# Kernel optimization log

Measured on AMD Instinct MI355X. Metric: run time of the kernel, lower is better.

The kernel has to match this reference:

```python
import jax, jax.numpy as jnp
import numpy as np

N_TOKEN = 267735
CUTOFF_ENDS = [0, 20000, 40000, 200000, N_TOKEN]
DIV_VAL = 4
D_MODEL = 1024
N_HEAD = 16
D_HEAD = 64
D_INNER = 4096
N_LAYER = 4
QLEN = 512
MLEN = 512
BSZ = 4
EPS = 1e-5


def setup_inputs() -> dict:
    key = jax.random.key(0)
    ks = iter(jax.random.split(key, 40))
    std = 0.02
    inp = {}
    inp["input_ids"] = jax.random.randint(next(ks), (BSZ, QLEN), 0, N_TOKEN)
    inp["mems"] = jax.random.normal(next(ks), (N_LAYER, MLEN, BSZ, D_MODEL), jnp.float32) * std
    # adaptive embedding tables + projections (div_val=4 buckets)
    for i in range(4):
        n = CUTOFF_ENDS[i + 1] - CUTOFF_ENDS[i]
        d = D_MODEL // DIV_VAL ** i
        inp[f"emb{i}"] = jax.random.normal(next(ks), (n, d), jnp.float32) * std
        inp[f"proj{i}"] = jax.random.normal(next(ks), (d, D_MODEL), jnp.float32) * std
    L = N_LAYER
    inp["qkv_w"] = jax.random.normal(next(ks), (L, D_MODEL, 3 * N_HEAD * D_HEAD), jnp.float32) * std
    inp["r_net_w"] = jax.random.normal(next(ks), (L, D_MODEL, N_HEAD * D_HEAD), jnp.float32) * std
    inp["o_w"] = jax.random.normal(next(ks), (L, N_HEAD * D_HEAD, D_MODEL), jnp.float32) * std
    inp["r_w_bias"] = jax.random.normal(next(ks), (L, N_HEAD, D_HEAD), jnp.float32) * std
    inp["r_r_bias"] = jax.random.normal(next(ks), (L, N_HEAD, D_HEAD), jnp.float32) * std
    inp["ln1_g"] = jnp.ones((L, D_MODEL), jnp.float32)
    inp["ln1_b"] = jnp.zeros((L, D_MODEL), jnp.float32)
    inp["ff_w1"] = jax.random.normal(next(ks), (L, D_MODEL, D_INNER), jnp.float32) * std
    inp["ff_b1"] = jnp.zeros((L, D_INNER), jnp.float32)
    inp["ff_w2"] = jax.random.normal(next(ks), (L, D_INNER, D_MODEL), jnp.float32) * std
    inp["ff_b2"] = jnp.zeros((L, D_MODEL), jnp.float32)
    inp["ln2_g"] = jnp.ones((L, D_MODEL), jnp.float32)
    inp["ln2_b"] = jnp.zeros((L, D_MODEL), jnp.float32)
    return inp


def _layer_norm(x, g, b):
    m = x.mean(-1, keepdims=True)
    v = ((x - m) ** 2).mean(-1, keepdims=True)
    return (x - m) * jax.lax.rsqrt(v + EPS) * g + b


def _rel_shift(x):
    # x: (qlen, klen, bsz, n_head)
    q, k, b, n = x.shape
    x = jnp.pad(x, ((0, 0), (1, 0), (0, 0), (0, 0)))
    x = x.reshape(k + 1, q, b, n)[1:]
    return x.reshape(q, k, b, n)


def _adaptive_embed(flat_ids, tables_projs):
    emb = jnp.zeros((flat_ids.shape[0], D_MODEL), jnp.float32)
    for i, (tab, proj) in enumerate(tables_projs):
        l, r = CUTOFF_ENDS[i], CUTOFF_ENDS[i + 1]
        mask = (flat_ids >= l) & (flat_ids < r)
        idx = jnp.clip(flat_ids - l, 0, r - l - 1)
        emb = emb + jnp.where(mask[:, None], tab[idx] @ proj, 0.0)
    return emb * (D_MODEL ** 0.5)


def _forward(input_ids, mems, tables_projs, qkv_w, r_net_w, o_w, r_w_bias, r_r_bias,
             ln1_g, ln1_b, ff_w1, ff_b1, ff_w2, ff_b2, ln2_g, ln2_b):
    ids = input_ids.T  # (qlen, bsz)
    word_emb = _adaptive_embed(ids.reshape(-1), tables_projs).reshape(QLEN, BSZ, D_MODEL)

    klen = MLEN + QLEN
    # masked positions == 1: future tokens only (strictly upper triangular over the q part)
    dec_attn_mask = jnp.concatenate(
        [jnp.zeros((QLEN, MLEN), jnp.float32), jnp.triu(jnp.ones((QLEN, QLEN), jnp.float32), 1)], axis=1
    )[:, :, None, None]  # (qlen, klen, 1, 1)

    pos_seq = jnp.arange(klen - 1, -1, -1, dtype=jnp.float32)
    inv_freq = 1.0 / (10000.0 ** (jnp.arange(0, D_MODEL, 2, dtype=jnp.float32) / D_MODEL))
    sin_inp = pos_seq[:, None] * inv_freq[None, :]
    pos_emb = jnp.concatenate([jnp.sin(sin_inp), jnp.cos(sin_inp)], axis=-1)  # (klen, d_model)

    scale = 1.0 / (D_HEAD ** 0.5)
    h = word_emb
    for l in range(N_LAYER):
        cat = jnp.concatenate([mems[l], h], axis=0)              # (klen, bsz, d)
        w_heads = cat @ qkv_w[l]                                  # (klen, bsz, 3*nh*dh)
        wq, wk, wv = jnp.split(w_heads, 3, axis=-1)
        q = wq[-QLEN:].reshape(QLEN, BSZ, N_HEAD, D_HEAD)
        k = wk.reshape(klen, BSZ, N_HEAD, D_HEAD)
        v = wv.reshape(klen, BSZ, N_HEAD, D_HEAD)
        rk = (pos_emb @ r_net_w[l]).reshape(klen, N_HEAD, D_HEAD)
        AC = jnp.einsum('ibnd,jbnd->ijbn', q + r_w_bias[l], k)
        BD = _rel_shift(jnp.einsum('ibnd,jnd->ijbn', q + r_r_bias[l], rk))
        score = (AC + BD) * scale
        score = score * (1.0 - dec_attn_mask) - 1e30 * dec_attn_mask
        prob = jax.nn.softmax(score, axis=1)
        attn_vec = jnp.einsum('ijbn,jbnd->ibnd', prob, v).reshape(QLEN, BSZ, N_HEAD * D_HEAD)
        h = _layer_norm(h + attn_vec @ o_w[l], ln1_g[l], ln1_b[l])
        core = jax.nn.relu(h @ ff_w1[l] + ff_b1[l]) @ ff_w2[l] + ff_b2[l]
        h = _layer_norm(h + core, ln2_g[l], ln2_b[l])
    return jnp.transpose(h, (1, 0, 2))  # (bsz, qlen, d_model)


def reference(input_ids, mems, emb0, proj0, emb1, proj1, emb2, proj2, emb3, proj3,
              qkv_w, r_net_w, o_w, r_w_bias, r_r_bias, ln1_g, ln1_b,
              ff_w1, ff_b1, ff_w2, ff_b2, ln2_g, ln2_b):
    tables_projs = [(emb0, proj0), (emb1, proj1), (emb2, proj2), (emb3, proj3)]
    return _forward(input_ids, mems, tables_projs, qkv_w, r_net_w, o_w, r_w_bias, r_r_bias,
                    ln1_g, ln1_b, ff_w1, ff_b1, ff_w2, ff_b2, ln2_g, ln2_b)
```

## Files before the change

kernel.cpp:

```cpp
#include <hip/hip_runtime.h>
#include <hip/hip_bf16.h>

typedef __attribute__((ext_vector_type(8))) short short8;
typedef __attribute__((ext_vector_type(4))) float f32x4;
typedef __hip_bfloat16 bf16;

#define QLEN 512
#define MLEN 512
#define KLEN 1024
#define BSZ  4
#define DM   1024
#define NH   16
#define DH   64
#define DI   4096
#define NL   4
#define KEMB 1408

__device__ __forceinline__ void gload16(const bf16* g, const void* l) {
  __builtin_amdgcn_global_load_lds(
      (const __attribute__((address_space(1))) void*)g,
      (__attribute__((address_space(3))) void*)l, 16, 0, 0);
}

__device__ __forceinline__ bf16 bits2bf(short s) { bf16 h; *(short*)&h = s; return h; }

__global__ __launch_bounds__(256) void embA_kernel(
    const int* __restrict__ ids,
    const float* __restrict__ e0, const float* __restrict__ e1,
    const float* __restrict__ e2, const float* __restrict__ e3,
    bf16* __restrict__ Aemb)
{
  const int t = blockIdx.x;
  const int q = t >> 2, b = t & 3;
  const int id = ids[b * QLEN + q];
  const float* tab; int d, off, koff;
  if (id < 20000)       { tab = e0; d = 1024; off = 0;      koff = 0; }
  else if (id < 40000)  { tab = e1; d = 256;  off = 20000;  koff = 1024; }
  else if (id < 200000) { tab = e2; d = 64;   off = 40000;  koff = 1280; }
  else                  { tab = e3; d = 16;   off = 200000; koff = 1344; }
  bf16* row = Aemb + (long)t * KEMB;
  const float* tr = tab + (long)(id - off) * d;
  for (int k = threadIdx.x; k < KEMB; k += 256) {
    const int kk = k - koff;
    float v = 0.f;
    if (kk >= 0 && kk < d) v = tr[kk];
    row[k] = __float2bfloat16(v);
  }
}

__global__ __launch_bounds__(256) void projT_kernel(
    const float* __restrict__ p0, const float* __restrict__ p1,
    const float* __restrict__ p2, const float* __restrict__ p3,
    bf16* __restrict__ out)
{
  __shared__ float t[32][33];
  const int k0 = blockIdx.x * 32, n0 = blockIdx.y * 32;
  const int nx = threadIdx.x & 31, ky = threadIdx.x >> 5;
#pragma unroll
  for (int p = 0; p < 4; ++p) {
    const int k = k0 + ky + p * 8;
    float v = 0.f;
    if (k < 1024)       v = p0[(long)k * 1024 + n0 + nx];
    else if (k < 1280)  v = p1[(long)(k - 1024) * 1024 + n0 + nx];
    else if (k < 1344)  v = p2[(long)(k - 1280) * 1024 + n0 + nx];
    else if (k < 1360)  v = p3[(long)(k - 1344) * 1024 + n0 + nx];
    t[ky + p * 8][nx] = v;
  }
  __syncthreads();
#pragma unroll
  for (int p = 0; p < 4; ++p)
    out[(long)(n0 + ky + p * 8) * KEMB + k0 + nx] = __float2bfloat16(t[nx][ky + p * 8]);
}

__global__ __launch_bounds__(256) void embsum_kernel(const float* __restrict__ part,
                                                     float* __restrict__ h, bf16* __restrict__ cat)
{
  const long i = ((long)blockIdx.x * 256 + threadIdx.x) * 4;
  const float4 a = *(const float4*)(part + i);
  const float4 b = *(const float4*)(part + 2097152 + i);
  float4 s; s.x = a.x + b.x; s.y = a.y + b.y; s.z = a.z + b.z; s.w = a.w + b.w;
  *(float4*)(h + i) = s;
  bf16* cr = cat + (long)2048 * 1024 + i;
  cr[0] = __float2bfloat16(s.x); cr[1] = __float2bfloat16(s.y);
  cr[2] = __float2bfloat16(s.z); cr[3] = __float2bfloat16(s.w);
}

__global__ __launch_bounds__(256) void posemb_kernel(bf16* __restrict__ pe)
{
  const int j = blockIdx.x;
  const float pos = (float)(KLEN - 1 - j);
  for (int i = threadIdx.x; i < DM / 2; i += 256) {
    const float freq = expf(-9.210340371976184f * ((float)(2 * i) / (float)DM));
    const float ang = pos * freq;
    pe[(long)j * DM + i]          = __float2bfloat16(sinf(ang));
    pe[(long)j * DM + DM / 2 + i] = __float2bfloat16(cosf(ang));
  }
}

__global__ __launch_bounds__(256) void wtrans_kernel(const float* __restrict__ in,
                                                     bf16* __restrict__ out, int R, int C)
{
  __shared__ float t[32][33];
  in  += (long)blockIdx.z * R * C;
  out += (long)blockIdx.z * R * C;
  const int c0 = blockIdx.x * 32, r0 = blockIdx.y * 32;
  const int cx = threadIdx.x & 31, ry = threadIdx.x >> 5;
#pragma unroll
  for (int p = 0; p < 4; ++p)
    t[ry + p * 8][cx] = in[(long)(r0 + ry + p * 8) * C + c0 + cx];
  __syncthreads();
#pragma unroll
  for (int p = 0; p < 4; ++p)
    out[(long)(c0 + ry + p * 8) * R + r0 + cx] = __float2bfloat16(t[cx][ry + p * 8]);
}

__global__ __launch_bounds__(256) void memsconv_kernel(const float* __restrict__ mems,
                                                       bf16* __restrict__ cat0)
{
  const long i = ((long)blockIdx.x * 256 + threadIdx.x) * 4;
  const long l = i >> 21, rem = i & ((1 << 21) - 1);
  const float4 v = *(const float4*)(mems + i);
  bf16* dst = cat0 + l * 4194304 + rem;
  dst[0] = __float2bfloat16(v.x); dst[1] = __float2bfloat16(v.y);
  dst[2] = __float2bfloat16(v.z); dst[3] = __float2bfloat16(v.w);
}

template<int BM, int BN>
__global__ __launch_bounds__(256) void gemm_bf16(
    const bf16* __restrict__ A, long aStrB, long aStrN, int lda,
    const bf16* __restrict__ B, long bStrB, long bStrN, int ldb,
    void* __restrict__ C, long cStrB, long cStrN, int ldc,
    int K, float scale, const float* __restrict__ bias, long biasStrB, long biasStrN,
    int flags, int zN, int zSplit, long cSplitStr)
{
  constexpr int RA = BM / 64, RB = BN / 64, FM = BM / 32, FN = BN / 32;
  __shared__ __align__(16) bf16 As[2][BM * 32];
  __shared__ __align__(16) bf16 Bs[2][BN * 32];
  const int zc = blockIdx.z % zSplit, zt = blockIdx.z / zSplit;
  const int zn = zt % zN, zb = zt / zN;
  A += (long)zb * aStrB + (long)zn * aStrN + (long)zc * K;
  B += (long)zb * bStrB + (long)zn * bStrN + (long)zc * K;
  const int tid = threadIdx.x, lane = tid & 63;
  const int w = tid >> 6, wr = w >> 1, wc = w & 1;
  const int m0 = blockIdx.y * BM, n0 = blockIdx.x * BN;
  const int l15 = lane & 15, l4 = lane >> 4;
  const int rowS = tid >> 2;
  const int cbS  = (tid & 3) * 16;
  const int swS  = cbS ^ (((rowS >> 1) & 3) << 4);
  const int wbase = w * 1024;
  const bf16* Ast = A + (size_t)(m0 + rowS) * lda + (swS >> 1);
  const bf16* Bst = B + (size_t)(n0 + rowS) * ldb + (swS >> 1);

#define STAGE_TILE(buf, kk)                                                       \
  {                                                                               \
    _Pragma("unroll")                                                             \
    for (int r = 0; r < RA; ++r)                                                  \
      gload16(Ast + (size_t)(r * 64) * lda + (kk), (char*)As[buf] + r * 4096 + wbase); \
    _Pragma("unroll")                                                             \
    for (int r = 0; r < RB; ++r)                                                  \
      gload16(Bst + (size_t)(r * 64) * ldb + (kk), (char*)Bs[buf] + r * 4096 + wbase); \
  }

  f32x4 acc[FM][FN] = {};
  STAGE_TILE(0, 0)
  asm volatile("s_waitcnt vmcnt(0)" ::: "memory");
  __syncthreads();
  int cur = 0;
  for (int k0 = 0; k0 < K; k0 += 32) {
    if (k0 + 32 < K) {
      if (cur == 0) STAGE_TILE(1, k0 + 32)
      else          STAGE_TILE(0, k0 + 32)
    }
    short8 af[FM], bfr[FN];
#pragma unroll
    for (int f = 0; f < FM; ++f) {
      const int row = wr * (BM / 2) + f * 16 + l15;
      af[f] = *(const short8*)((char*)As[cur] + row * 64 + ((16 * l4) ^ (((row >> 1) & 3) << 4)));
    }
#pragma unroll
    for (int f = 0; f < FN; ++f) {
      const int row = wc * (BN / 2) + f * 16 + l15;
      bfr[f] = *(const short8*)((char*)Bs[cur] + row * 64 + ((16 * l4) ^ (((row >> 1) & 3) << 4)));
    }
#pragma unroll
    for (int fm = 0; fm < FM; ++fm)
#pragma unroll
      for (int fn = 0; fn < FN; ++fn)
        acc[fm][fn] = __builtin_amdgcn_mfma_f32_16x16x32_bf16(af[fm], bfr[fn], acc[fm][fn], 0, 0, 0);
    asm volatile("s_waitcnt vmcnt(0)" ::: "memory");
    __syncthreads();
    cur ^= 1;
  }
#undef STAGE_TILE
  const int outbf = flags & 1, relu = flags & 4;
#pragma unroll
  for (int fm = 0; fm < FM; ++fm) {
#pragma unroll
    for (int fn = 0; fn < FN; ++fn) {
      const int col = n0 + wc * (BN / 2) + fn * 16 + l15;
      const int rw0 = m0 + wr * (BM / 2) + fm * 16 + l4 * 4;
      const float bv = (bias && zc == 0) ? bias[(size_t)zb * biasStrB + (size_t)zn * biasStrN + col] : 0.f;
#pragma unroll
      for (int r = 0; r < 4; ++r) {
        float v = (acc[fm][fn][r] + bv) * scale;
        if (relu) v = fmaxf(v, 0.f);
        const int row = rw0 + r;
        const size_t cOff = (size_t)zb * cStrB + (size_t)zn * cStrN + (size_t)zc * cSplitStr;
        if (outbf) {
          ((bf16*)C + cOff)[(size_t)row * ldc + col] = __float2bfloat16(v);
        } else {
          ((float*)C + cOff)[(size_t)row * ldc + col] = v;
        }
      }
    }
  }
}

__global__ __launch_bounds__(256) void vt_kernel(const bf16* __restrict__ wh,
                                                 bf16* __restrict__ vt, bf16* __restrict__ kb)
{
  const int bn = blockIdx.y, b = bn >> 4, n = bn & 15;
  const int j0 = blockIdx.x * 64;
  __shared__ bf16 t[64][72];
  const bf16* src = wh + (size_t)b * 3072 + 2048 + n * 64;
  const bf16* ksrc = wh + (size_t)b * 3072 + 1024 + n * 64;
  bf16* kdst = kb + (size_t)bn * 65536;
  const int tid = threadIdx.x;
#pragma unroll
  for (int r = 0; r < 16; ++r) {
    const int jl = r * 4 + (tid >> 6), d = tid & 63;
    t[jl][d] = src[(size_t)(j0 + jl) * 12288 + d];
    kdst[(size_t)(j0 + jl) * 64 + d] = ksrc[(size_t)(j0 + jl) * 12288 + d];
  }
  __syncthreads();
  bf16* dst = vt + (size_t)bn * 65536 + (size_t)j0 * 64;
#pragma unroll
  for (int r = 0; r < 16; ++r) {
    const int d = r * 4 + (tid >> 6), j = tid & 63;
    dst[(size_t)d * 64 + j] = t[j][d];
  }
}

__global__ __launch_bounds__(256) void rkpack_kernel(const bf16* __restrict__ rkb,
                                                     bf16* __restrict__ rkn)
{
  const int ln = blockIdx.y, l = ln >> 4, n = ln & 15;
  const int p0 = blockIdx.x * 64;
  const int d = threadIdx.x & 63, pr = threadIdx.x >> 6;
  const bf16* src = rkb + (size_t)l * 1048576 + n * 64 + d;
  bf16* dst = rkn + (size_t)ln * 65536 + d;
#pragma unroll
  for (int r = 0; r < 16; ++r) {
    const int p = p0 + r * 4 + pr;
    dst[(size_t)p * 64] = src[(size_t)p * 1024];
  }
}

__global__ __launch_bounds__(256) void fattn_kernel(
    const bf16* __restrict__ wh,
    const bf16* __restrict__ kb,
    const bf16* __restrict__ rkn_l,
    const bf16* __restrict__ vt,
    const float* __restrict__ rwb,
    const float* __restrict__ rrb,
    float* __restrict__ po, float* __restrict__ pm, float* __restrict__ pl)
{
  const int bn = blockIdx.x, b = bn >> 4, n = bn & 15;
  const int q0 = blockIdx.y * 64;
  const int ck = blockIdx.z;
  const int tid = threadIdx.x, w = tid >> 6, lane = tid & 63;
  const int l15 = lane & 15, l4 = lane >> 4;
  __shared__ bf16 Tl[4][16][84];
  __shared__ bf16 Pl[4][16][72];

  short8 qa[2], qb[2];
  {
    const bf16* qp = wh + (size_t)(2048 + b) * 3072 + (size_t)(q0 + 16 * w + l15) * 12288 + n * 64;
#pragma unroll
    for (int kk = 0; kk < 2; ++kk) {
      const short8 qv = *(const short8*)(qp + kk * 32 + 8 * l4);
      const float* wv = rwb + n * 64 + kk * 32 + 8 * l4;
      const float* rv = rrb + n * 64 + kk * 32 + 8 * l4;
      short8 a, c;
#pragma unroll
      for (int e = 0; e < 8; ++e) {
        const float q = __bfloat162float(bits2bf(qv[e]));
        const bf16 ab = __float2bfloat16((q + wv[e]) * 0.125f);
        const bf16 cb = __float2bfloat16((q + rv[e]) * 0.125f);
        a[e] = *(const short*)&ab;  c[e] = *(const short*)&cb;
      }
      qa[kk] = a; qb[kk] = c;
    }
  }

  const bf16* kbase = kb + (size_t)bn * 65536;
  const bf16* rbase = rkn_l + (size_t)n * 65536;
  const bf16* vbase = vt + (size_t)bn * 65536;
  const int ntiles = 9 + (q0 >> 6);
  const int pb0 = -q0 + 496 - 16 * w;

  f32x4 accO[4] = {};
  float mrow[4] = { -1e30f, -1e30f, -1e30f, -1e30f };
  float lrow[4] = { 0.f, 0.f, 0.f, 0.f };

  for (int t = ck; t < ntiles; t += 4) {
    const int j0 = t * 64;
    f32x4 S[4] = {};
#pragma unroll
    for (int fn = 0; fn < 4; ++fn)
#pragma unroll
      for (int kk = 0; kk < 2; ++kk) {
        const short8 kf = *(const short8*)(kbase + (size_t)(j0 + 16 * fn + l15) * 64 + kk * 32 + 8 * l4);
        S[fn] = __builtin_amdgcn_mfma_f32_16x16x32_bf16(qa[kk], kf, S[fn], 0, 0, 0);
      }
    {
      f32x4 T[5] = {};
#pragma unroll
      for (int ftl = 0; ftl < 5; ++ftl) {
        const int p = pb0 + j0 + 16 * ftl + l15;
#pragma unroll
        for (int kk = 0; kk < 2; ++kk) {
          const short8 rf = *(const short8*)(rbase + (size_t)p * 64 + kk * 32 + 8 * l4);
          T[ftl] = __builtin_amdgcn_mfma_f32_16x16x32_bf16(qb[kk], rf, T[ftl], 0, 0, 0);
        }
      }
#pragma unroll
      for (int ftl = 0; ftl < 5; ++ftl)
#pragma unroll
        for (int r = 0; r < 4; ++r)
          Tl[w][4 * l4 + r][16 * ftl + l15] = __float2bfloat16(T[ftl][r]);
    }
    const bool fullvalid = (j0 + 63) <= (512 + q0);
    float sv[4][4];
#pragma unroll
    for (int fn = 0; fn < 4; ++fn)
#pragma unroll
      for (int r = 0; r < 4; ++r) {
        const int il = 4 * l4 + r;
        const float tshift = __bfloat162float(Tl[w][il][16 * fn + l15 + 15 - il]);
        const float s = S[fn][r] + tshift;
        const bool valid = fullvalid || (j0 + 16 * fn + l15 - 512 <= q0 + 16 * w + il);
        sv[fn][r] = valid ? s : -1e30f;
      }
#pragma unroll
    for (int r = 0; r < 4; ++r) {
      float m4 = fmaxf(fmaxf(sv[0][r], sv[1][r]), fmaxf(sv[2][r], sv[3][r]));
      m4 = fmaxf(m4, __shfl_xor(m4, 1));
      m4 = fmaxf(m4, __shfl_xor(m4, 2));
      m4 = fmaxf(m4, __shfl_xor(m4, 4));
      m4 = fmaxf(m4, __shfl_xor(m4, 8));
      const float mn = fmaxf(mrow[r], m4);
      const float alpha = expf(mrow[r] - mn);
      mrow[r] = mn;
      float ps = 0.f;
#pragma unroll
      for (int fn = 0; fn < 4; ++fn) {
        sv[fn][r] = expf(sv[fn][r] - mn);
        ps += sv[fn][r];
      }
      ps += __shfl_xor(ps, 1);
      ps += __shfl_xor(ps, 2);
      ps += __shfl_xor(ps, 4);
      ps += __shfl_xor(ps, 8);
      lrow[r] = lrow[r] * alpha + ps;
#pragma unroll
      for (int fd = 0; fd < 4; ++fd) accO[fd][r] *= alpha;
    }
#pragma unroll
    for (int fn = 0; fn < 4; ++fn)
#pragma unroll
      for (int r = 0; r < 4; ++r)
        Pl[w][4 * l4 + r][16 * fn + l15] = __float2bfloat16(sv[fn][r]);
    short8 pa[2];
    pa[0] = *(const short8*)&Pl[w][l15][8 * l4];
    pa[1] = *(const short8*)&Pl[w][l15][32 + 8 * l4];
    const bf16* vtile = vbase + (size_t)j0 * 64;
#pragma unroll
    for (int fd = 0; fd < 4; ++fd)
#pragma unroll
      for (int kk = 0; kk < 2; ++kk) {
        const short8 vf = *(const short8*)(vtile + (size_t)(16 * fd + l15) * 64 + kk * 32 + 8 * l4);
        accO[fd] = __builtin_amdgcn_mfma_f32_16x16x32_bf16(pa[kk], vf, accO[fd], 0, 0, 0);
      }
  }
  const int cb = ck * 64 + bn;
  float* pob = po + (size_t)cb * 512 * 64;
#pragma unroll
  for (int fd = 0; fd < 4; ++fd)
#pragma unroll
    for (int r = 0; r < 4; ++r) {
      const int row = q0 + 16 * w + 4 * l4 + r;
      pob[(size_t)row * 64 + 16 * fd + l15] = accO[fd][r];
    }
  if (l15 == 0) {
#pragma unroll
    for (int r = 0; r < 4; ++r) {
      const int row = q0 + 16 * w + 4 * l4 + r;
      pm[(size_t)cb * 512 + row] = mrow[r];
      pl[(size_t)cb * 512 + row] = lrow[r];
    }
  }
}

__global__ __launch_bounds__(256) void fmerge_kernel(
    const float* __restrict__ po, const float* __restrict__ pm,
    const float* __restrict__ pl, bf16* __restrict__ av)
{
  const long i = ((long)blockIdx.x * 256 + threadIdx.x) * 4;
  const long bnq = i >> 6;
  const int d4 = (int)(i & 63);
  const int bn = (int)(bnq >> 9), q = (int)(bnq & 511);
  const int b = bn >> 4, n = bn & 15;
  float mv[4], lv[4];
#pragma unroll
  for (int c = 0; c < 4; ++c) { mv[c] = pm[c * 32768 + bnq]; lv[c] = pl[c * 32768 + bnq]; }
  const float m = fmaxf(fmaxf(mv[0], mv[1]), fmaxf(mv[2], mv[3]));
  float wv[4], den = 0.f;
#pragma unroll
  for (int c = 0; c < 4; ++c) { wv[c] = expf(mv[c] - m); den += wv[c] * lv[c]; }
  const float inv = 1.f / den;
  float4 o = { 0.f, 0.f, 0.f, 0.f };
#pragma unroll
  for (int c = 0; c < 4; ++c) {
    const float4 oc = *(const float4*)(po + (size_t)c * 2097152 + bnq * 64 + d4);
    o.x += wv[c] * oc.x; o.y += wv[c] * oc.y; o.z += wv[c] * oc.z; o.w += wv[c] * oc.w;
  }
  bf16* dst = av + (size_t)(q * 4 + b) * 1024 + n * 64 + d4;
  dst[0] = __float2bfloat16(o.x * inv);
  dst[1] = __float2bfloat16(o.y * inv);
  dst[2] = __float2bfloat16(o.z * inv);
  dst[3] = __float2bfloat16(o.w * inv);
}

__global__ __launch_bounds__(256) void add_ln_kernel(
    float* __restrict__ h,
    const float* __restrict__ x0, const float* __restrict__ x1,
    const float* __restrict__ g, const float* __restrict__ bb, bf16* __restrict__ cat)
{
  float* hr = h + (long)blockIdx.x * DM;
  const long o = (long)blockIdx.x * DM;
  bf16* cr = cat + (long)(2048 + blockIdx.x) * DM;
  const int tid = threadIdx.x;
  __shared__ float red[256];
  float v0 = hr[tid]       + x0[o + tid]       + x1[o + tid];
  float v1 = hr[tid + 256] + x0[o + tid + 256] + x1[o + tid + 256];
  float v2 = hr[tid + 512] + x0[o + tid + 512] + x1[o + tid + 512];
  float v3 = hr[tid + 768] + x0[o + tid + 768] + x1[o + tid + 768];
  red[tid] = v0 + v1 + v2 + v3; __syncthreads();
  for (int off = 128; off; off >>= 1) { if (tid < off) red[tid] += red[tid + off]; __syncthreads(); }
  const float mean = red[0] * (1.f / DM); __syncthreads();
  const float d0 = v0 - mean, d1 = v1 - mean, d2 = v2 - mean, d3 = v3 - mean;
  red[tid] = d0 * d0 + d1 * d1 + d2 * d2 + d3 * d3; __syncthreads();
  for (int off = 128; off; off >>= 1) { if (tid < off) red[tid] += red[tid + off]; __syncthreads(); }
  const float inv = rsqrtf(red[0] * (1.f / DM) + 1e-5f);
  const float o0 = d0 * inv * g[tid]       + bb[tid];
  const float o1 = d1 * inv * g[tid + 256] + bb[tid + 256];
  const float o2 = d2 * inv * g[tid + 512] + bb[tid + 512];
  const float o3 = d3 * inv * g[tid + 768] + bb[tid + 768];
  hr[tid]       = o0;  cr[tid]       = __float2bfloat16(o0);
  hr[tid + 256] = o1;  cr[tid + 256] = __float2bfloat16(o1);
  hr[tid + 512] = o2;  cr[tid + 512] = __float2bfloat16(o2);
  hr[tid + 768] = o3;  cr[tid + 768] = __float2bfloat16(o3);
}

__global__ __launch_bounds__(256) void out_kernel(const float* __restrict__ h, float* __restrict__ out)
{
  const int t = blockIdx.x, q = t >> 2, b = t & 3;
  const float* hr = h + (long)t * DM;
  float* orow = out + ((long)b * QLEN + q) * DM;
  for (int s = 0; s < 4; ++s) orow[threadIdx.x + 256 * s] = hr[threadIdx.x + 256 * s];
}

extern "C" void kernel_launch(void* const* d_in, const int* in_sizes, int n_in,
                              void* d_out, int out_size, void* d_ws, size_t ws_size,
                              hipStream_t stream)
{
  const int*   ids  = (const int*)d_in[0];
  const float* mems = (const float*)d_in[1];
  const float* e0 = (const float*)d_in[2]; const float* p0 = (const float*)d_in[3];
  const float* e1 = (const float*)d_in[4]; const float* p1 = (const float*)d_in[5];
  const float* e2 = (const float*)d_in[6]; const float* p2 = (const float*)d_in[7];
  const float* e3 = (const float*)d_in[8]; const float* p3 = (const float*)d_in[9];
  const float* qkvw = (const float*)d_in[10];
  const float* rnet = (const float*)d_in[11];
  const float* ow   = (const float*)d_in[12];
  const float* rwb  = (const float*)d_in[13];
  const float* rrb  = (const float*)d_in[14];
  const float* ln1g = (const float*)d_in[15];
  const float* ln1b = (const float*)d_in[16];
  const float* fw1  = (const float*)d_in[17];
  const float* fb1  = (const float*)d_in[18];
  const float* fw2  = (const float*)d_in[19];
  const float* fb2  = (const float*)d_in[20];
  const float* ln2g = (const float*)d_in[21];
  const float* ln2b = (const float*)d_in[22];
  float* out = (float*)d_out;

  char* p = (char*)d_ws;
  float* h    = (float*)p;            p += (size_t)2048 * 1024 * 4;
  bf16*  cat0 = (bf16*)p;             p += (size_t)5 * 4096 * 1024 * 2;
  bf16*  pe   = (bf16*)p;             p += (size_t)1024 * 1024 * 2;
  bf16*  rkb  = (bf16*)p;             p += (size_t)4 * 1024 * 1024 * 2;
  bf16*  rkn  = (bf16*)p;             p += (size_t)(4 * 16 * 1024 * 64 + 8192) * 2;
  bf16*  wh   = (bf16*)p;             p += (size_t)4096 * 3072 * 2;
  bf16*  vt   = (bf16*)p;             p += (size_t)64 * 64 * 1024 * 2;
  bf16*  kb   = (bf16*)p;             p += (size_t)64 * 1024 * 64 * 2;
  bf16*  qkvT = (bf16*)p;             p += (size_t)4 * 3072 * 1024 * 2;
  bf16*  rnT  = (bf16*)p;             p += (size_t)4 * 1024 * 1024 * 2;
  bf16*  oT   = (bf16*)p;             p += (size_t)4 * 1024 * 1024 * 2;
  bf16*  f1T  = (bf16*)p;             p += (size_t)4 * 4096 * 1024 * 2;
  bf16*  f2T  = (bf16*)p;             p += (size_t)4 * 4096 * 1024 * 2;
  bf16*  mid  = (bf16*)p;
  float* partE= (float*)p;
  p += (size_t)4 * 16 * 512 * 1024 * 2;
  bf16*  Aemb = (bf16*)p;
  bf16*  projT= (bf16*)(p + (size_t)2048 * KEMB * 2);
  float* partP= (float*)p;
  float* po   = (float*)p;
  float* pm   = (float*)(p + (size_t)32 * 1024 * 1024);
  float* pl   = (float*)(p + (size_t)33 * 1024 * 1024);
  p += (size_t)4 * 16 * 512 * 1024 * 2;
  bf16*  av   = (bf16*)p;             p += (size_t)2048 * 1024 * 2;

  embA_kernel<<<2048, 256, 0, stream>>>(ids, e0, e1, e2, e3, Aemb);
  projT_kernel<<<dim3(KEMB / 32, 32), 256, 0, stream>>>(p0, p1, p2, p3, projT);
  gemm_bf16<128, 64><<<dim3(16, 16, 2), 256, 0, stream>>>(
      Aemb, 0, 0, KEMB, projT, 0, 0, KEMB, partE, 0, 0, 1024,
      KEMB / 2, 32.f, nullptr, 0, 0, 0, 1, 2, 2097152);
  embsum_kernel<<<2048, 256, 0, stream>>>(partE, h, cat0);
  posemb_kernel<<<1024, 256, 0, stream>>>(pe);
  memsconv_kernel<<<8192, 256, 0, stream>>>(mems, cat0);

  wtrans_kernel<<<dim3(96, 32, 4), 256, 0, stream>>>(qkvw, qkvT, DM, 3072);
  wtrans_kernel<<<dim3(32, 32, 4), 256, 0, stream>>>(rnet, rnT, DM, DM);
  wtrans_kernel<<<dim3(32, 32, 4), 256, 0, stream>>>(ow, oT, DM, DM);
  wtrans_kernel<<<dim3(128, 32, 4), 256, 0, stream>>>(fw1, f1T, DM, DI);
  wtrans_kernel<<<dim3(32, 128, 4), 256, 0, stream>>>(fw2, f2T, DI, DM);

  gemm_bf16<128, 128><<<dim3(8, 8, 4), 256, 0, stream>>>(
      pe, 0, 0, 1024, rnT, 1048576, 0, 1024, rkb, 1048576, 0, 1024,
      1024, 1.f, nullptr, 0, 0, 1, 1, 1, 0);
  rkpack_kernel<<<dim3(16, 64), 256, 0, stream>>>(rkb, rkn);

  for (int l = 0; l < NL; ++l) {
    bf16* catl = cat0 + (size_t)l * 4194304;
    gemm_bf16<128, 128><<<dim3(24, 32, 1), 256, 0, stream>>>(
        catl, 0, 0, 1024, qkvT + (size_t)l * 3145728, 0, 0, 1024, wh, 0, 0, 3072,
        1024, 1.f, nullptr, 0, 0, 1, 1, 1, 0);

    vt_kernel<<<dim3(16, 64), 256, 0, stream>>>(wh, vt, kb);

    fattn_kernel<<<dim3(64, 8, 4), 256, 0, stream>>>(
        wh, kb, rkn + (size_t)l * 1048576, vt,
        rwb + l * NH * DH, rrb + l * NH * DH, po, pm, pl);
    fmerge_kernel<<<2048, 256, 0, stream>>>(po, pm, pl, av);

    gemm_bf16<128, 64><<<dim3(16, 16, 2), 256, 0, stream>>>(
        av, 0, 0, 1024, oT + (size_t)l * 1048576, 0, 0, 1024, partP, 0, 0, 1024,
        512, 1.f, nullptr, 0, 0, 0, 1, 2, 2097152);
    add_ln_kernel<<<2048, 256, 0, stream>>>(h, partP, partP + 2097152,
                                            ln1g + l * DM, ln1b + l * DM, catl);

    gemm_bf16<128, 128><<<dim3(32, 16, 1), 256, 0, stream>>>(
        catl + (size_t)2048 * 1024, 0, 0, 1024, f1T + (size_t)l * 4194304, 0, 0, 1024,
        mid, 0, 0, 4096, 1024, 1.f, fb1 + (size_t)l * DI, 0, 0, 1 | 4, 1, 1, 0);
    gemm_bf16<128, 64><<<dim3(16, 16, 2), 256, 0, stream>>>(
        mid, 0, 0, 4096, f2T + (size_t)l * 4194304, 0, 0, 4096, partP, 0, 0, 1024,
        2048, 1.f, fb2 + (size_t)l * DM, 0, 0, 0, 1, 2, 2097152);
    add_ln_kernel<<<2048, 256, 0, stream>>>(h, partP, partP + 2097152,
                                            ln2g + l * DM, ln2b + l * DM,
                                            cat0 + (size_t)(l + 1) * 4194304);
  }

  out_kernel<<<2048, 256, 0, stream>>>(h, out);
}
```

Measured before the change: 1.159 ms.

## Stage K, V and relative-position tiles in swizzled LDS for attention kernel

The attention kernel now cooperatively loads each 64-row K tile, V tile and 128-row relative-position key tile into LDS with direct global-to-LDS loads and an XOR swizzle. All four waves then read their MFMA operands from shared memory instead of each wave loading them from global memory. This is meant to cut redundant global/L2 traffic, since the four waves previously reloaded the same K/V rows and overlapping R rows. It adds two block barriers and a full vmcnt wait per tile with no double-buffering, so load latency is exposed rather than overlapped.

```diff
diff --git a/kernel.cpp b/kernel.cpp
--- a/kernel.cpp
+++ b/kernel.cpp
@@ -270,6 +270,9 @@
   const int ck = blockIdx.z;
   const int tid = threadIdx.x, w = tid >> 6, lane = tid & 63;
   const int l15 = lane & 15, l4 = lane >> 4;
+  __shared__ __align__(16) bf16 Ks[64 * 64];
+  __shared__ __align__(16) bf16 Vs[64 * 64];
+  __shared__ __align__(16) bf16 Rs[128 * 64];
   __shared__ bf16 Tl[4][16][84];
   __shared__ bf16 Pl[4][16][72];
 
@@ -299,28 +302,58 @@
   const int ntiles = 9 + (q0 >> 6);
   const int pb0 = -q0 + 496 - 16 * w;
 
+  const int stRow0 = tid >> 3;
+  const int stColb = (tid & 7) * 16;
+  const int wbase = w * 1024;
+  const int srd = (l15 & 7) << 4;
+
   f32x4 accO[4] = {};
   float mrow[4] = { -1e30f, -1e30f, -1e30f, -1e30f };
   float lrow[4] = { 0.f, 0.f, 0.f, 0.f };
 
   for (int t = ck; t < ntiles; t += 4) {
     const int j0 = t * 64;
+    const int pstart = j0 - q0 + 448;
+    __syncthreads();
+    {
+#pragma unroll
+      for (int r = 0; r < 2; ++r) {
+        const int row = r * 32 + stRow0;
+        gload16(kbase + (size_t)(j0 + row) * 64 + ((stColb ^ ((row & 7) << 4)) >> 1),
+                (char*)Ks + r * 4096 + wbase);
+      }
+#pragma unroll
+      for (int r = 0; r < 2; ++r) {
+        const int row = r * 32 + stRow0;
+        gload16(vbase + (size_t)j0 * 64 + (size_t)row * 64 + ((stColb ^ ((row & 7) << 4)) >> 1),
+                (char*)Vs + r * 4096 + wbase);
+      }
+#pragma unroll
+      for (int r = 0; r < 4; ++r) {
+        const int row = r * 32 + stRow0;
+        gload16(rbase + (size_t)(pstart + row) * 64 + ((stColb ^ ((row & 7) << 4)) >> 1),
+                (char*)Rs + r * 4096 + wbase);
+      }
+    }
+    asm volatile("s_waitcnt vmcnt(0)" ::: "memory");
+    __syncthreads();
+
     f32x4 S[4] = {};
 #pragma unroll
     for (int fn = 0; fn < 4; ++fn)
 #pragma unroll
       for (int kk = 0; kk < 2; ++kk) {
-        const short8 kf = *(const short8*)(kbase + (size_t)(j0 + 16 * fn + l15) * 64 + kk * 32 + 8 * l4);
+        const short8 kf = *(const short8*)((char*)Ks + (16 * fn + l15) * 128 + ((kk * 64 + 16 * l4) ^ srd));
         S[fn] = __builtin_amdgcn_mfma_f32_16x16x32_bf16(qa[kk], kf, S[fn], 0, 0, 0);
       }
     {
       f32x4 T[5] = {};
 #pragma unroll
       for (int ftl = 0; ftl < 5; ++ftl) {
-        const int p = pb0 + j0 + 16 * ftl + l15;
+        const int rrow = (3 - w) * 16 + 16 * ftl + l15;
 #pragma unroll
         for (int kk = 0; kk < 2; ++kk) {
-          const short8 rf = *(const short8*)(rbase + (size_t)p * 64 + kk * 32 + 8 * l4);
+          const short8 rf = *(const short8*)((char*)Rs + rrow * 128 + ((kk * 64 + 16 * l4) ^ srd));
           T[ftl] = __builtin_amdgcn_mfma_f32_16x16x32_bf16(qb[kk], rf, T[ftl], 0, 0, 0);
         }
       }
@@ -374,12 +407,11 @@
     short8 pa[2];
     pa[0] = *(const short8*)&Pl[w][l15][8 * l4];
     pa[1] = *(const short8*)&Pl[w][l15][32 + 8 * l4];
-    const bf16* vtile = vbase + (size_t)j0 * 64;
 #pragma unroll
     for (int fd = 0; fd < 4; ++fd)
 #pragma unroll
       for (int kk = 0; kk < 2; ++kk) {
-        const short8 vf = *(const short8*)(vtile + (size_t)(16 * fd + l15) * 64 + kk * 32 + 8 * l4);
+        const short8 vf = *(const short8*)((char*)Vs + (16 * fd + l15) * 128 + ((kk * 64 + 16 * l4) ^ srd));
         accO[fd] = __builtin_amdgcn_mfma_f32_16x16x32_bf16(pa[kk], vf, accO[fd], 0, 0, 0);
       }
   }
```

New measurement: 980.8 us. -15.3%, faster.

## Stage K, V and R tiles in swizzled double-buffered LDS with async loads

Applied to the files above, without the earlier changes.

The fused relative-attention kernel now copies each 64-key K tile, V tile and a 128-row relative-position R tile into shared memory with global_load_lds. The buffers are double-buffered so the next tile is prefetched while the current one is computed. MFMA operand fragments are read from LDS through an XOR swizzle instead of each wave loading the same rows directly from global memory. This removes redundant per-wave global reads and hides load latency, and the separate T and P scratch arrays are merged into one to save LDS. The cost is higher LDS use, which may lower occupancy, plus a block-wide barrier and vmcnt wait at every tile.

```diff
diff --git a/kernel.cpp b/kernel.cpp
--- a/kernel.cpp
+++ b/kernel.cpp
@@ -270,8 +270,10 @@
   const int ck = blockIdx.z;
   const int tid = threadIdx.x, w = tid >> 6, lane = tid & 63;
   const int l15 = lane & 15, l4 = lane >> 4;
-  __shared__ bf16 Tl[4][16][84];
-  __shared__ bf16 Pl[4][16][72];
+  __shared__ __align__(16) bf16 Ks[2][64 * 64];
+  __shared__ __align__(16) bf16 Vs[2][64 * 64];
+  __shared__ __align__(16) bf16 Rs[2][128 * 64];
+  __shared__ bf16 TP[4][16][84];
 
   short8 qa[2], qb[2];
   {
@@ -297,30 +299,66 @@
   const bf16* rbase = rkn_l + (size_t)n * 65536;
   const bf16* vbase = vt + (size_t)bn * 65536;
   const int ntiles = 9 + (q0 >> 6);
-  const int pb0 = -q0 + 496 - 16 * w;
+
+  const int stRow0 = tid >> 3;
+  const int stColb = (tid & 7) * 16;
+  const int wbase = w * 1024;
+  const int srd = (l15 & 7) << 4;
+
+#define FA_STAGE(buf, j0s)                                                                   \
+  {                                                                                          \
+    const int psrt = (j0s) - q0 + 448;                                                       \
+    _Pragma("unroll")                                                                        \
+    for (int r = 0; r < 2; ++r) {                                                            \
+      const int row = r * 32 + stRow0;                                                       \
+      gload16(kbase + (size_t)((j0s) + row) * 64 + ((stColb ^ ((row & 7) << 4)) >> 1),       \
+              (char*)Ks + (buf) * 8192 + r * 4096 + wbase);                                  \
+    }                                                                                        \
+    _Pragma("unroll")                                                                        \
+    for (int r = 0; r < 2; ++r) {                                                            \
+      const int row = r * 32 + stRow0;                                                       \
+      gload16(vbase + (size_t)(j0s) * 64 + (size_t)row * 64 + ((stColb ^ ((row & 7) << 4)) >> 1), \
+              (char*)Vs + (buf) * 8192 + r * 4096 + wbase);                                  \
+    }                                                                                        \
+    _Pragma("unroll")                                                                        \
+    for (int r = 0; r < 4; ++r) {                                                            \
+      const int row = r * 32 + stRow0;                                                       \
+      gload16(rbase + (size_t)(psrt + row) * 64 + ((stColb ^ ((row & 7) << 4)) >> 1),        \
+              (char*)Rs + (buf) * 16384 + r * 4096 + wbase);                                 \
+    }                                                                                        \
+  }
 
   f32x4 accO[4] = {};
   float mrow[4] = { -1e30f, -1e30f, -1e30f, -1e30f };
   float lrow[4] = { 0.f, 0.f, 0.f, 0.f };
 
+  FA_STAGE(0, ck * 64)
+  asm volatile("s_waitcnt vmcnt(0)" ::: "memory");
+  __syncthreads();
+  int cur = 0;
+
   for (int t = ck; t < ntiles; t += 4) {
     const int j0 = t * 64;
+    if (t + 4 < ntiles) {
+      if (cur == 0) FA_STAGE(1, (t + 4) * 64)
+      else          FA_STAGE(0, (t + 4) * 64)
+    }
     f32x4 S[4] = {};
 #pragma unroll
     for (int fn = 0; fn < 4; ++fn)
 #pragma unroll
       for (int kk = 0; kk < 2; ++kk) {
-        const short8 kf = *(const short8*)(kbase + (size_t)(j0 + 16 * fn + l15) * 64 + kk * 32 + 8 * l4);
+        const short8 kf = *(const short8*)((char*)Ks + cur * 8192 + (16 * fn + l15) * 128 + ((kk * 64 + 16 * l4) ^ srd));
         S[fn] = __builtin_amdgcn_mfma_f32_16x16x32_bf16(qa[kk], kf, S[fn], 0, 0, 0);
       }
     {
       f32x4 T[5] = {};
 #pragma unroll
       for (int ftl = 0; ftl < 5; ++ftl) {
-        const int p = pb0 + j0 + 16 * ftl + l15;
+        const int rrow = (3 - w) * 16 + 16 * ftl + l15;
 #pragma unroll
         for (int kk = 0; kk < 2; ++kk) {
-          const short8 rf = *(const short8*)(rbase + (size_t)p * 64 + kk * 32 + 8 * l4);
+          const short8 rf = *(const short8*)((char*)Rs + cur * 16384 + rrow * 128 + ((kk * 64 + 16 * l4) ^ srd));
           T[ftl] = __builtin_amdgcn_mfma_f32_16x16x32_bf16(qb[kk], rf, T[ftl], 0, 0, 0);
         }
       }
@@ -328,7 +366,7 @@
       for (int ftl = 0; ftl < 5; ++ftl)
 #pragma unroll
         for (int r = 0; r < 4; ++r)
-          Tl[w][4 * l4 + r][16 * ftl + l15] = __float2bfloat16(T[ftl][r]);
+          TP[w][4 * l4 + r][16 * ftl + l15] = __float2bfloat16(T[ftl][r]);
     }
     const bool fullvalid = (j0 + 63) <= (512 + q0);
     float sv[4][4];
@@ -337,7 +375,7 @@
 #pragma unroll
       for (int r = 0; r < 4; ++r) {
         const int il = 4 * l4 + r;
-        const float tshift = __bfloat162float(Tl[w][il][16 * fn + l15 + 15 - il]);
+        const float tshift = __bfloat162float(TP[w][il][16 * fn + l15 + 15 - il]);
         const float s = S[fn][r] + tshift;
         const bool valid = fullvalid || (j0 + 16 * fn + l15 - 512 <= q0 + 16 * w + il);
         sv[fn][r] = valid ? s : -1e30f;
@@ -370,19 +408,22 @@
     for (int fn = 0; fn < 4; ++fn)
 #pragma unroll
       for (int r = 0; r < 4; ++r)
-        Pl[w][4 * l4 + r][16 * fn + l15] = __float2bfloat16(sv[fn][r]);
+        TP[w][4 * l4 + r][16 * fn + l15] = __float2bfloat16(sv[fn][r]);
     short8 pa[2];
-    pa[0] = *(const short8*)&Pl[w][l15][8 * l4];
-    pa[1] = *(const short8*)&Pl[w][l15][32 + 8 * l4];
-    const bf16* vtile = vbase + (size_t)j0 * 64;
+    pa[0] = *(const short8*)&TP[w][l15][8 * l4];
+    pa[1] = *(const short8*)&TP[w][l15][32 + 8 * l4];
 #pragma unroll
     for (int fd = 0; fd < 4; ++fd)
 #pragma unroll
       for (int kk = 0; kk < 2; ++kk) {
-        const short8 vf = *(const short8*)(vtile + (size_t)(16 * fd + l15) * 64 + kk * 32 + 8 * l4);
+        const short8 vf = *(const short8*)((char*)Vs + cur * 8192 + (16 * fd + l15) * 128 + ((kk * 64 + 16 * l4) ^ srd));
         accO[fd] = __builtin_amdgcn_mfma_f32_16x16x32_bf16(pa[kk], vf, accO[fd], 0, 0, 0);
       }
-  }
+    asm volatile("s_waitcnt vmcnt(0)" ::: "memory");
+    __syncthreads();
+    cur ^= 1;
+  }
+#undef FA_STAGE
   const int cb = ck * 64 + bn;
   float* pob = po + (size_t)cb * 512 * 64;
 #pragma unroll
```

Result: faster. 996.4 us (-14.0%).
